# Optimization experiments

Hardware: AMD Instinct MI355X
Metric: run time of the kernel (lower is better)

## Reference

```python
import jax, jax.numpy as jnp
import numpy as np

N, R, D, K = 2048, 64, 64, 512  # batch, n_roles, filler_embed_dim, n_fillers
LAMBDA_VQ, LAMBDA_COMMIT, LAMBDA_ORTH = 1.0, 0.5, 0.0


def setup_inputs() -> dict:
    key = jax.random.key(0)
    k1, k2 = jax.random.split(key)
    soft_fillers = jax.random.normal(k1, (N, R, D), dtype=jnp.float32)
    weight = jax.random.normal(k2, (K, D), dtype=jnp.float32)  # codebook rows
    return {"soft_fillers": soft_fillers, "weight": weight}


def _nearest(x, w):
    # x: [M, D], w: [K, D] -> nearest codebook rows + indices
    d = (jnp.sum(x * x, axis=-1, keepdims=True)
         - 2.0 * (x @ w.T)
         + jnp.sum(w * w, axis=-1))          # [M, K]
    idx = jnp.argmin(d, axis=-1)              # [M]
    return w[idx], idx                        # gather: [M, D]


def reference(soft_fillers, weight):
    flat = soft_fillers.reshape(-1, D)        # [N*R, D]

    # Path 1: weight_sg=True -> weight detached, straight-through to input
    q_sg_flat, idx = _nearest(flat, jax.lax.stop_gradient(weight))
    q_sg_flat = flat + jax.lax.stop_gradient(q_sg_flat - flat)

    # Path 2: input detached -> gradient flows to weight via gather
    q_flat, _ = _nearest(jax.lax.stop_gradient(flat), weight)

    q_sg = q_sg_flat.reshape(N, R, D)
    q = q_flat.reshape(N, R, D)
    filler_idxs = idx.reshape(N, R)

    # vq loss: mean over (N, D) of L2-norm over roles of elementwise-squared diff
    t_vq = (q - jax.lax.stop_gradient(soft_fillers)) ** 2          # [N, R, D]
    vq_loss = jnp.mean(jnp.sqrt(jnp.sum(t_vq * t_vq, axis=1)))
    t_c = (jax.lax.stop_gradient(q) - soft_fillers) ** 2
    commit_loss = jnp.mean(jnp.sqrt(jnp.sum(t_c * t_c, axis=1)))

    # semi-orthogonality penalty on weight.t() (rows of codebook): ||W^T W - I||_F
    gram = weight.T @ weight                                        # [D, D]
    orth_penalty = jnp.linalg.norm(gram - jnp.eye(D, dtype=weight.dtype))

    total_loss = (LAMBDA_VQ * vq_loss + LAMBDA_COMMIT * commit_loss
                  + LAMBDA_ORTH * orth_penalty)

    filler_rank = jnp.linalg.matrix_rank(weight).astype(jnp.float32)

    return (total_loss, vq_loss, commit_loss, orth_penalty, filler_rank,
            q_sg, q, filler_idxs)
```

## Files before the change

kernel.cpp:

```cpp
#include <hip/hip_runtime.h>
#include <math.h>

#define N_ 2048
#define R_ 64
#define D_ 64
#define K_ 512
#define M_ (N_*R_)
#define TAU 0.012f
#define CHK 0.012f

#define WN_OFF   16
#define GRAM_OFF 1024
#define WBF_BYTE 32768
#define WS_NEED  163840

typedef __attribute__((ext_vector_type(8))) short s16x8;
typedef __attribute__((ext_vector_type(4))) float f32x4;

static __device__ __forceinline__ unsigned short f2bf(float f) {
    unsigned u = __float_as_uint(f);
    u += 0x7FFFu + ((u >> 16) & 1u);
    return (unsigned short)(u >> 16);
}
static __device__ __forceinline__ float bf2f(unsigned short h) {
    return __uint_as_float(((unsigned)h) << 16);
}

static __device__ __forceinline__ int xs_byte(int r, int q) {
    return r * 256 + (q >> 3) * 128 + (((q & 7) ^ (r & 7)) * 16);
}

static __device__ __forceinline__ void split8(const float* vv, s16x8& ph, s16x8& pl) {
#pragma unroll
    for (int j = 0; j < 8; ++j) {
        const unsigned short hb = f2bf(vv[j]);
        ph[j] = (short)hb;
        pl[j] = (short)f2bf(vv[j] - bf2f(hb));
    }
}

static __device__ __forceinline__ void nt_store4(float* p, float x0, float x1, float x2, float x3) {
    f32x4 v = {x0, x1, x2, x3};
    __builtin_nontemporal_store(v, (f32x4*)p);
}

__global__ void k_pre(const float* __restrict__ w, float* __restrict__ ws, int pre) {
    const int b = blockIdx.x, t = threadIdx.x;
    if (b < 64) {
        __shared__ float red[4][64];
        const int i = b, j = t & 63, kg = t >> 6;
        float s = 0.f;
        for (int k = kg * 128; k < kg * 128 + 128; ++k)
            s = fmaf(w[k * 64 + i], w[k * 64 + j], s);
        red[kg][j] = s;
        __syncthreads();
        if (t < 64)
            ws[GRAM_OFF + i * 64 + t] = red[0][t] + red[1][t] + red[2][t] + red[3][t];
    } else if (b < 66) {
        const int code = (b - 64) * 256 + t;
        const float4* wr = (const float4*)(w + code * 64);
        float s = 0.f;
#pragma unroll
        for (int i = 0; i < 16; ++i) {
            float4 v = wr[i];
            s += v.x * v.x + v.y * v.y + v.z * v.z + v.w * v.w;
        }
        ws[WN_OFF + code] = s;
        if (b == 64 && t == 0) ws[0] = 0.f;
    } else {
        if (!pre) return;
        const int code = (b - 66) * 256 + t;
        char* whi = (char*)ws + WBF_BYTE;
        char* wlo = whi + 65536;
        const int c = code >> 6, rr = code & 63;
        const int nt = rr >> 4, lr = rr & 15;
        for (int kg = 0; kg < 8; ++kg) {
            float4 v0 = *(const float4*)(w + code * 64 + kg * 8);
            float4 v1 = *(const float4*)(w + code * 64 + kg * 8 + 4);
            const float vv[8] = {v0.x, v0.y, v0.z, v0.w, v1.x, v1.y, v1.z, v1.w};
            s16x8 ph, pl;
            split8(vv, ph, pl);
            const int s = kg >> 2, g = kg & 3, l = g * 16 + lr;
            const int off = (((c * 2 + s) * 4 + nt) << 10) + l * 16;
            *(s16x8*)(whi + off) = ph;
            *(s16x8*)(wlo + off) = pl;
        }
    }
}

template<bool PRE>
__global__ __launch_bounds__(256, 2) void k_argmin(
    const float* __restrict__ x, const float* __restrict__ w,
    float* __restrict__ ws, float* __restrict__ out)
{
    __shared__ __align__(16) float xs[8192];
    __shared__ __align__(16) float redw[2][4][64];
    __shared__ float fb1[128], fb2[128];
    __shared__ int   ridx[128];
    __shared__ int   ulist[128];
    __shared__ int   nunc;

    const int t = threadIdx.x;
    const int l = t & 63, wid = t >> 6;
    const int g = l >> 4, lr = l & 15;
    const long brow = (long)blockIdx.x * 128;
    const float* wn_g = ws + WN_OFF;
    const char* whi = (const char*)ws + WBF_BYTE;
    const char* wlo = whi + 65536;

    if (t == 0) nunc = 0;

#pragma unroll
    for (int ii = 0; ii < 8; ++ii) {
        const int gid = ii * 256 + t;
        const int r = gid >> 4, qq = gid & 15;
        const float4 v = *(const float4*)(x + (brow + r) * 64 + qq * 4);
        *(float4*)((char*)xs + xs_byte(r, qq)) = v;
    }
    __syncthreads();

    s16x8 ah[2][2], al[2][2];
#pragma unroll
    for (int mt = 0; mt < 2; ++mt) {
        const int row = wid * 32 + mt * 16 + lr;
#pragma unroll
        for (int s = 0; s < 2; ++s) {
            const int kg = s * 4 + g;
            const float4 v0 = *(const float4*)((const char*)xs + xs_byte(row, kg * 2));
            const float4 v1 = *(const float4*)((const char*)xs + xs_byte(row, kg * 2 + 1));
            const float vv[8] = {v0.x, v0.y, v0.z, v0.w, v1.x, v1.y, v1.z, v1.w};
            split8(vv, ah[mt][s], al[mt][s]);
        }
    }

    float b1[2][4], b2[2][4]; int i1[2][4];
#pragma unroll
    for (int mt = 0; mt < 2; ++mt)
#pragma unroll
        for (int j = 0; j < 4; ++j) { b1[mt][j] = 3.4e38f; b2[mt][j] = 3.4e38f; i1[mt][j] = 0; }

    s16x8 pbh[2][4], pbl[2][4];
    float4 pv0[2][4], pv1[2][4];
    f32x4 acc[2][4];

    auto issue = [&](int h, int par) {
        const int c = h >> 1, half = h & 1;
#pragma unroll
        for (int s = 0; s < 2; ++s)
#pragma unroll
            for (int nth = 0; nth < 2; ++nth) {
                const int nt = half * 2 + nth, idx = s * 2 + nth;
                if constexpr (PRE) {
                    const int off = (((c * 2 + s) * 4 + nt) << 10) + l * 16;
                    pbh[par][idx] = *(const s16x8*)(whi + off);
                    pbl[par][idx] = *(const s16x8*)(wlo + off);
                } else {
                    const int crow = c * 64 + nt * 16 + lr;
                    const float* src = w + (long)crow * 64 + (s * 4 + g) * 8;
                    pv0[par][idx] = *(const float4*)src;
                    pv1[par][idx] = *(const float4*)(src + 4);
                }
            }
    };

    auto compute = [&](int h, int par) {
        const int c = h >> 1, half = h & 1;
        if (half == 0) {
            const f32x4 z = {0.f, 0.f, 0.f, 0.f};
#pragma unroll
            for (int mt = 0; mt < 2; ++mt)
#pragma unroll
                for (int nt = 0; nt < 4; ++nt) acc[mt][nt] = z;
        }
#pragma unroll
        for (int s = 0; s < 2; ++s)
#pragma unroll
            for (int nth = 0; nth < 2; ++nth) {
                const int nt = half * 2 + nth, idx = s * 2 + nth;
                s16x8 BH, BL;
                if constexpr (PRE) {
                    BH = pbh[par][idx]; BL = pbl[par][idx];
                } else {
                    const float4 v0 = pv0[par][idx], v1 = pv1[par][idx];
                    const float vv[8] = {v0.x, v0.y, v0.z, v0.w, v1.x, v1.y, v1.z, v1.w};
                    split8(vv, BH, BL);
                }
#pragma unroll
                for (int mt = 0; mt < 2; ++mt) {
                    acc[mt][nt] = __builtin_amdgcn_mfma_f32_16x16x32_bf16(ah[mt][s], BH, acc[mt][nt], 0, 0, 0);
                    acc[mt][nt] = __builtin_amdgcn_mfma_f32_16x16x32_bf16(al[mt][s], BH, acc[mt][nt], 0, 0, 0);
                    acc[mt][nt] = __builtin_amdgcn_mfma_f32_16x16x32_bf16(ah[mt][s], BL, acc[mt][nt], 0, 0, 0);
                }
            }
        if (half == 1) {
#pragma unroll
            for (int nt = 0; nt < 4; ++nt) {
                const int code = c * 64 + nt * 16 + lr;
                const float wnv = wn_g[code];
#pragma unroll
                for (int mt = 0; mt < 2; ++mt)
#pragma unroll
                    for (int j = 0; j < 4; ++j) {
                        const float sv = fmaf(-2.f, acc[mt][nt][j], wnv);
                        if (sv < b1[mt][j]) { b2[mt][j] = b1[mt][j]; b1[mt][j] = sv; i1[mt][j] = code; }
                        else if (sv < b2[mt][j]) b2[mt][j] = sv;
                    }
            }
        }
    };

    issue(0, 0);
#pragma unroll
    for (int h = 0; h < 16; ++h) {
        if (h < 15) issue(h + 1, (h + 1) & 1);
        compute(h, h & 1);
    }

#pragma unroll
    for (int m = 1; m < 16; m <<= 1) {
#pragma unroll
        for (int mt = 0; mt < 2; ++mt)
#pragma unroll
            for (int j = 0; j < 4; ++j) {
                const float ov1 = __shfl_xor(b1[mt][j], m, 64);
                const int   oi1 = __shfl_xor(i1[mt][j], m, 64);
                const float ov2 = __shfl_xor(b2[mt][j], m, 64);
                const float nb2 = fminf(fminf(b2[mt][j], ov2), fmaxf(b1[mt][j], ov1));
                if (ov1 < b1[mt][j] || (ov1 == b1[mt][j] && oi1 < i1[mt][j])) {
                    b1[mt][j] = ov1; i1[mt][j] = oi1;
                }
                b2[mt][j] = nb2;
            }
    }
    if (lr == 0) {
#pragma unroll
        for (int mt = 0; mt < 2; ++mt)
#pragma unroll
            for (int j = 0; j < 4; ++j) {
                const int ro = wid * 32 + mt * 16 + g * 4 + j;
                ridx[ro] = i1[mt][j];
                fb1[ro] = b1[mt][j];
                fb2[ro] = b2[mt][j];
            }
    }
    __syncthreads();

    {
        const int r = t >> 1, sub = t & 1;
        const int ci = ridx[r];
        const float* wrow = w + (long)ci * 64 + sub * 32;
        float dot = 0.f;
#pragma unroll
        for (int p = 0; p < 8; ++p) {
            const float4 xv = *(const float4*)((const char*)xs + xs_byte(r, sub * 8 + p));
            const float4 wv = *(const float4*)(wrow + p * 4);
            dot = fmaf(xv.x, wv.x, dot);
            dot = fmaf(xv.y, wv.y, dot);
            dot = fmaf(xv.z, wv.z, dot);
            dot = fmaf(xv.w, wv.w, dot);
        }
        dot += __shfl_xor(dot, 1, 64);
        if (sub == 0) {
            const float sex = fmaf(-2.f, dot, wn_g[ci]);
            const bool unc = ((fb2[r] - fb1[r]) < TAU) || (fabsf(sex - fb1[r]) > CHK);
            if (unc) { const int p = atomicAdd(&nunc, 1); ulist[p] = r; }
        }
    }
    __syncthreads();

    const int nu = nunc;
    if (nu > 0) {
        for (int e = wid; e < nu; e += 4) {
            const int r = ulist[e];
            float bv = 3.4e38f; int bi = 0;
            for (int cc = 0; cc < 8; ++cc) {
                const int code = cc * 64 + l;
                const float* wrow = w + (long)code * 64;
                float dot = 0.f;
#pragma unroll
                for (int p = 0; p < 16; ++p) {
                    const float4 xv = *(const float4*)((const char*)xs + xs_byte(r, p));
                    const float4 wv = *(const float4*)(wrow + p * 4);
                    dot = fmaf(xv.x, wv.x, dot);
                    dot = fmaf(xv.y, wv.y, dot);
                    dot = fmaf(xv.z, wv.z, dot);
                    dot = fmaf(xv.w, wv.w, dot);
                }
                const float sv = fmaf(-2.f, dot, wn_g[code]);
                if (sv < bv) { bv = sv; bi = code; }
            }
#pragma unroll
            for (int m = 1; m < 64; m <<= 1) {
                const float ov = __shfl_xor(bv, m, 64);
                const int   oi = __shfl_xor(bi, m, 64);
                if (ov < bv || (ov == bv && oi < bi)) { bv = ov; bi = oi; }
            }
            if (l == 0) ridx[r] = bi;
        }
    }
    __syncthreads();

    float* q_sg = out + 5;
    float* q    = out + 5 + (long)M_ * 64;
    float* fidx = out + 5 + 2L * M_ * 64;
    const int qq = t & 15, ry = t >> 4;
    float4 va = {0.f, 0.f, 0.f, 0.f}, vb = {0.f, 0.f, 0.f, 0.f};
#pragma unroll
    for (int ii = 0; ii < 8; ++ii) {
        const int r = ii * 16 + ry;
        const int ci = ridx[r];
        const float4 wv4 = *(const float4*)(w + (long)ci * 64 + qq * 4);
        const float4 xv4 = *(const float4*)((const char*)xs + xs_byte(r, qq));
        const long off = (brow + r) * 64 + qq * 4;
        nt_store4(q_sg + off, wv4.x, wv4.y, wv4.z, wv4.w);
        nt_store4(q + off,    wv4.x, wv4.y, wv4.z, wv4.w);
        float4 p;
        p.x = (wv4.x - xv4.x) * (wv4.x - xv4.x);
        p.y = (wv4.y - xv4.y) * (wv4.y - xv4.y);
        p.z = (wv4.z - xv4.z) * (wv4.z - xv4.z);
        p.w = (wv4.w - xv4.w) * (wv4.w - xv4.w);
        float4 p2;
        p2.x = p.x * p.x; p2.y = p.y * p.y; p2.z = p.z * p.z; p2.w = p.w * p.w;
        if (ii < 4) {
            va.x += p2.x; va.y += p2.y; va.z += p2.z; va.w += p2.w;
        } else {
            vb.x += p2.x; vb.y += p2.y; vb.z += p2.z; vb.w += p2.w;
        }
    }
#pragma unroll
    for (int m = 16; m < 64; m <<= 1) {
        va.x += __shfl_xor(va.x, m, 64); va.y += __shfl_xor(va.y, m, 64);
        va.z += __shfl_xor(va.z, m, 64); va.w += __shfl_xor(va.w, m, 64);
        vb.x += __shfl_xor(vb.x, m, 64); vb.y += __shfl_xor(vb.y, m, 64);
        vb.z += __shfl_xor(vb.z, m, 64); vb.w += __shfl_xor(vb.w, m, 64);
    }
    if (l < 16) {
        *(float4*)&redw[0][wid][l * 4] = va;
        *(float4*)&redw[1][wid][l * 4] = vb;
    }
    if (t < 128) __builtin_nontemporal_store((float)ridx[t], fidx + brow + t);
    __syncthreads();

    if (t < 128) {
        const int n = t >> 6, d = t & 63;
        const float s = redw[n][0][d] + redw[n][1][d] + redw[n][2][d] + redw[n][3][d];
        float v = sqrtf(s);
#pragma unroll
        for (int m = 1; m < 64; m <<= 1) v += __shfl_xor(v, m, 64);
        if (d == 0) atomicAdd(ws + 0, v);
    }
}

__global__ void k_final(const float* __restrict__ ws, float* __restrict__ out)
{
    __shared__ float g[64][65];
    __shared__ float osum[4];
    __shared__ float tol;
    const int t = threadIdx.x;
    float oacc = 0.f;
    for (int i = t; i < 4096; i += 256) {
        const int r = i >> 6, cl = i & 63;
        const float gv = ws[GRAM_OFF + i];
        g[r][cl] = gv;
        const float p = gv - (r == cl ? 1.f : 0.f);
        oacc = fmaf(p, p, oacc);
    }
#pragma unroll
    for (int m = 1; m < 64; m <<= 1) oacc += __shfl_xor(oacc, m, 64);
    if ((t & 63) == 0) osum[t >> 6] = oacc;
    __syncthreads();

    if (t == 0) {
        float maxd = 0.f;
        for (int i = 0; i < 64; ++i) maxd = fmaxf(maxd, fabsf(g[i][i]));
        tol = maxd * 1e-7f + 1e-30f;
    }
    __syncthreads();

    int rank = 0;
    const int j = t & 63, rq = t >> 6;
    for (int s = 0; s < 64; ++s) {
        const float p = g[s][s];
        const bool ok = fabsf(p) > tol;
        if (ok) {
            rank++;
            if (j > s) {
                const float rp = 1.f / p;
                const float gsj = g[s][j];
                for (int r = s + 1 + rq; r < 64; r += 4)
                    g[r][j] = fmaf(-(g[r][s] * rp), gsj, g[r][j]);
            }
        }
        __syncthreads();
    }

    if (t == 0) {
        const float vq = ws[0] / (float)(N_ * D_);
        const float orth = sqrtf(osum[0] + osum[1] + osum[2] + osum[3]);
        out[0] = 1.5f * vq;
        out[1] = vq;
        out[2] = vq;
        out[3] = orth;
        out[4] = (float)rank;
    }
}

extern "C" void kernel_launch(void* const* d_in, const int* in_sizes, int n_in,
                              void* d_out, int out_size, void* d_ws, size_t ws_size,
                              hipStream_t stream) {
    const float* x = (const float*)d_in[0];
    const float* w = (const float*)d_in[1];
    float* out = (float*)d_out;
    float* ws  = (float*)d_ws;
    const int pre = (ws_size >= (size_t)WS_NEED) ? 1 : 0;

    hipLaunchKernelGGL(k_pre, dim3(68), dim3(256), 0, stream, w, ws, pre);
    if (pre)
        hipLaunchKernelGGL((k_argmin<true>),  dim3(1024), dim3(256), 0, stream, x, w, ws, out);
    else
        hipLaunchKernelGGL((k_argmin<false>), dim3(1024), dim3(256), 0, stream, x, w, ws, out);
    hipLaunchKernelGGL(k_final, dim3(1), dim3(256), 0, stream, ws, out);
}
```

Measured before the change: 164.5 us.

## Fuse gram and finalize into argmin kernel via last-block completion counter

The gram-matrix computation moves out of the pre-pass into 64 extra blocks of the main argmin kernel, and the separate single-block final kernel is folded in. Its work now runs in whichever block is last to increment a global atomic counter. This cuts one launch and shrinks the pre-pass to 4 blocks, so the gram work overlaps with the argmin work. In exchange the gram matrix is no longer ready early, every block adds a threadfence and atomic at its end, and the serial rank elimination runs inside a heavy kernel's tail block.

```diff
diff --git a/kernel.cpp b/kernel.cpp
--- a/kernel.cpp
+++ b/kernel.cpp
@@ -9,6 +9,10 @@
 #define TAU 0.012f
 #define CHK 0.012f
 
+#define GRAMB 64
+#define ARGB  1024
+#define TOTB  (GRAMB + ARGB)
+
 #define WN_OFF   16
 #define GRAM_OFF 1024
 #define WBF_BYTE 32768
@@ -46,18 +50,8 @@
 
 __global__ void k_pre(const float* __restrict__ w, float* __restrict__ ws, int pre) {
     const int b = blockIdx.x, t = threadIdx.x;
-    if (b < 64) {
-        __shared__ float red[4][64];
-        const int i = b, j = t & 63, kg = t >> 6;
-        float s = 0.f;
-        for (int k = kg * 128; k < kg * 128 + 128; ++k)
-            s = fmaf(w[k * 64 + i], w[k * 64 + j], s);
-        red[kg][j] = s;
-        __syncthreads();
-        if (t < 64)
-            ws[GRAM_OFF + i * 64 + t] = red[0][t] + red[1][t] + red[2][t] + red[3][t];
-    } else if (b < 66) {
-        const int code = (b - 64) * 256 + t;
+    if (b < 2) {
+        const int code = b * 256 + t;
         const float4* wr = (const float4*)(w + code * 64);
         float s = 0.f;
 #pragma unroll
@@ -66,10 +60,10 @@
             s += v.x * v.x + v.y * v.y + v.z * v.z + v.w * v.w;
         }
         ws[WN_OFF + code] = s;
-        if (b == 64 && t == 0) ws[0] = 0.f;
+        if (b == 0 && t == 0) { ws[0] = 0.f; ((int*)ws)[8] = 0; }
     } else {
         if (!pre) return;
-        const int code = (b - 66) * 256 + t;
+        const int code = (b - 2) * 256 + t;
         char* whi = (char*)ws + WBF_BYTE;
         char* wlo = whi + 65536;
         const int c = code >> 6, rr = code & 63;
@@ -89,279 +83,301 @@
 }
 
 template<bool PRE>
-__global__ __launch_bounds__(256, 2) void k_argmin(
+__global__ __launch_bounds__(256, 2) void k_main(
     const float* __restrict__ x, const float* __restrict__ w,
     float* __restrict__ ws, float* __restrict__ out)
 {
     __shared__ __align__(16) float xs[8192];
     __shared__ __align__(16) float redw[2][4][64];
     __shared__ float fb1[128], fb2[128];
-    __shared__ int   ridx[128];
+    __shared__ int   sridx[128];
     __shared__ int   ulist[128];
     __shared__ int   nunc;
+    __shared__ int   lastflag;
 
     const int t = threadIdx.x;
     const int l = t & 63, wid = t >> 6;
     const int g = l >> 4, lr = l & 15;
-    const long brow = (long)blockIdx.x * 128;
     const float* wn_g = ws + WN_OFF;
     const char* whi = (const char*)ws + WBF_BYTE;
     const char* wlo = whi + 65536;
 
-    if (t == 0) nunc = 0;
-
-#pragma unroll
-    for (int ii = 0; ii < 8; ++ii) {
-        const int gid = ii * 256 + t;
-        const int r = gid >> 4, qq = gid & 15;
-        const float4 v = *(const float4*)(x + (brow + r) * 64 + qq * 4);
-        *(float4*)((char*)xs + xs_byte(r, qq)) = v;
-    }
+    if (blockIdx.x < GRAMB) {
+        const int i = blockIdx.x, j = t & 63, kg = t >> 6;
+        float s = 0.f;
+#pragma unroll 4
+        for (int k = kg * 128; k < kg * 128 + 128; ++k)
+            s = fmaf(w[k * 64 + i], w[k * 64 + j], s);
+        float* red = xs;
+        red[kg * 64 + j] = s;
+        __syncthreads();
+        if (t < 64)
+            ws[GRAM_OFF + i * 64 + t] = red[t] + red[64 + t] + red[128 + t] + red[192 + t];
+    } else {
+        const int bid = blockIdx.x - GRAMB;
+        const long brow = (long)bid * 128;
+
+        if (t == 0) nunc = 0;
+
+#pragma unroll
+        for (int ii = 0; ii < 8; ++ii) {
+            const int gid = ii * 256 + t;
+            const int r = gid >> 4, qq = gid & 15;
+            const float4 v = *(const float4*)(x + (brow + r) * 64 + qq * 4);
+            *(float4*)((char*)xs + xs_byte(r, qq)) = v;
+        }
+        __syncthreads();
+
+        s16x8 ah[2][2], al[2][2];
+#pragma unroll
+        for (int mt = 0; mt < 2; ++mt) {
+            const int row = wid * 32 + mt * 16 + lr;
+#pragma unroll
+            for (int s = 0; s < 2; ++s) {
+                const int kg = s * 4 + g;
+                const float4 v0 = *(const float4*)((const char*)xs + xs_byte(row, kg * 2));
+                const float4 v1 = *(const float4*)((const char*)xs + xs_byte(row, kg * 2 + 1));
+                const float vv[8] = {v0.x, v0.y, v0.z, v0.w, v1.x, v1.y, v1.z, v1.w};
+                split8(vv, ah[mt][s], al[mt][s]);
+            }
+        }
+
+        float b1[2][4], b2[2][4]; int i1[2][4];
+#pragma unroll
+        for (int mt = 0; mt < 2; ++mt)
+#pragma unroll
+            for (int j = 0; j < 4; ++j) { b1[mt][j] = 3.4e38f; b2[mt][j] = 3.4e38f; i1[mt][j] = 0; }
+
+        s16x8 pbh[2][4], pbl[2][4];
+        float4 pv0[2][4], pv1[2][4];
+        f32x4 acc[2][4];
+
+        auto issue = [&](int h, int par) {
+            const int c = h >> 1, half = h & 1;
+#pragma unroll
+            for (int s = 0; s < 2; ++s)
+#pragma unroll
+                for (int nth = 0; nth < 2; ++nth) {
+                    const int nt = half * 2 + nth, idx = s * 2 + nth;
+                    if constexpr (PRE) {
+                        const int off = (((c * 2 + s) * 4 + nt) << 10) + l * 16;
+                        pbh[par][idx] = *(const s16x8*)(whi + off);
+                        pbl[par][idx] = *(const s16x8*)(wlo + off);
+                    } else {
+                        const int crow = c * 64 + nt * 16 + lr;
+                        const float* src = w + (long)crow * 64 + (s * 4 + g) * 8;
+                        pv0[par][idx] = *(const float4*)src;
+                        pv1[par][idx] = *(const float4*)(src + 4);
+                    }
+                }
+        };
+
+        auto compute = [&](int h, int par) {
+            const int c = h >> 1, half = h & 1;
+            if (half == 0) {
+                const f32x4 z = {0.f, 0.f, 0.f, 0.f};
+#pragma unroll
+                for (int mt = 0; mt < 2; ++mt)
+#pragma unroll
+                    for (int nt = 0; nt < 4; ++nt) acc[mt][nt] = z;
+            }
+#pragma unroll
+            for (int s = 0; s < 2; ++s)
+#pragma unroll
+                for (int nth = 0; nth < 2; ++nth) {
+                    const int nt = half * 2 + nth, idx = s * 2 + nth;
+                    s16x8 BH, BL;
+                    if constexpr (PRE) {
+                        BH = pbh[par][idx]; BL = pbl[par][idx];
+                    } else {
+                        const float4 v0 = pv0[par][idx], v1 = pv1[par][idx];
+                        const float vv[8] = {v0.x, v0.y, v0.z, v0.w, v1.x, v1.y, v1.z, v1.w};
+                        split8(vv, BH, BL);
+                    }
+#pragma unroll
+                    for (int mt = 0; mt < 2; ++mt) {
+                        acc[mt][nt] = __builtin_amdgcn_mfma_f32_16x16x32_bf16(ah[mt][s], BH, acc[mt][nt], 0, 0, 0);
+                        acc[mt][nt] = __builtin_amdgcn_mfma_f32_16x16x32_bf16(al[mt][s], BH, acc[mt][nt], 0, 0, 0);
+                        acc[mt][nt] = __builtin_amdgcn_mfma_f32_16x16x32_bf16(ah[mt][s], BL, acc[mt][nt], 0, 0, 0);
+                    }
+                }
+            if (half == 1) {
+#pragma unroll
+                for (int nt = 0; nt < 4; ++nt) {
+                    const int code = c * 64 + nt * 16 + lr;
+                    const float wnv = wn_g[code];
+#pragma unroll
+                    for (int mt = 0; mt < 2; ++mt)
+#pragma unroll
+                        for (int j = 0; j < 4; ++j) {
+                            const float sv = fmaf(-2.f, acc[mt][nt][j], wnv);
+                            if (sv < b1[mt][j]) { b2[mt][j] = b1[mt][j]; b1[mt][j] = sv; i1[mt][j] = code; }
+                            else if (sv < b2[mt][j]) b2[mt][j] = sv;
+                        }
+                }
+            }
+        };
+
+        issue(0, 0);
+#pragma unroll
+        for (int h = 0; h < 16; ++h) {
+            if (h < 15) issue(h + 1, (h + 1) & 1);
+            compute(h, h & 1);
+        }
+
+#pragma unroll
+        for (int m = 1; m < 16; m <<= 1) {
+#pragma unroll
+            for (int mt = 0; mt < 2; ++mt)
+#pragma unroll
+                for (int j = 0; j < 4; ++j) {
+                    const float ov1 = __shfl_xor(b1[mt][j], m, 64);
+                    const int   oi1 = __shfl_xor(i1[mt][j], m, 64);
+                    const float ov2 = __shfl_xor(b2[mt][j], m, 64);
+                    const float nb2 = fminf(fminf(b2[mt][j], ov2), fmaxf(b1[mt][j], ov1));
+                    if (ov1 < b1[mt][j] || (ov1 == b1[mt][j] && oi1 < i1[mt][j])) {
+                        b1[mt][j] = ov1; i1[mt][j] = oi1;
+                    }
+                    b2[mt][j] = nb2;
+                }
+        }
+        if (lr == 0) {
+#pragma unroll
+            for (int mt = 0; mt < 2; ++mt)
+#pragma unroll
+                for (int j = 0; j < 4; ++j) {
+                    const int ro = wid * 32 + mt * 16 + g * 4 + j;
+                    sridx[ro] = i1[mt][j];
+                    fb1[ro] = b1[mt][j];
+                    fb2[ro] = b2[mt][j];
+                }
+        }
+        __syncthreads();
+
+        {
+            const int r = t >> 1, sub = t & 1;
+            const int ci = sridx[r];
+            const float* wrow = w + (long)ci * 64 + sub * 32;
+            float dot = 0.f;
+#pragma unroll
+            for (int p = 0; p < 8; ++p) {
+                const float4 xv = *(const float4*)((const char*)xs + xs_byte(r, sub * 8 + p));
+                const float4 wv = *(const float4*)(wrow + p * 4);
+                dot = fmaf(xv.x, wv.x, dot);
+                dot = fmaf(xv.y, wv.y, dot);
+                dot = fmaf(xv.z, wv.z, dot);
+                dot = fmaf(xv.w, wv.w, dot);
+            }
+            dot += __shfl_xor(dot, 1, 64);
+            if (sub == 0) {
+                const float sex = fmaf(-2.f, dot, wn_g[ci]);
+                const bool unc = ((fb2[r] - fb1[r]) < TAU) || (fabsf(sex - fb1[r]) > CHK);
+                if (unc) { const int p = atomicAdd(&nunc, 1); ulist[p] = r; }
+            }
+        }
+        __syncthreads();
+
+        const int nu = nunc;
+        if (nu > 0) {
+            for (int e = wid; e < nu; e += 4) {
+                const int r = ulist[e];
+                float bv = 3.4e38f; int bi = 0;
+                for (int cc = 0; cc < 8; ++cc) {
+                    const int code = cc * 64 + l;
+                    const float* wrow = w + (long)code * 64;
+                    float dot = 0.f;
+#pragma unroll
+                    for (int p = 0; p < 16; ++p) {
+                        const float4 xv = *(const float4*)((const char*)xs + xs_byte(r, p));
+                        const float4 wv = *(const float4*)(wrow + p * 4);
+                        dot = fmaf(xv.x, wv.x, dot);
+                        dot = fmaf(xv.y, wv.y, dot);
+                        dot = fmaf(xv.z, wv.z, dot);
+                        dot = fmaf(xv.w, wv.w, dot);
+                    }
+                    const float sv = fmaf(-2.f, dot, wn_g[code]);
+                    if (sv < bv) { bv = sv; bi = code; }
+                }
+#pragma unroll
+                for (int m = 1; m < 64; m <<= 1) {
+                    const float ov = __shfl_xor(bv, m, 64);
+                    const int   oi = __shfl_xor(bi, m, 64);
+                    if (ov < bv || (ov == bv && oi < bi)) { bv = ov; bi = oi; }
+                }
+                if (l == 0) sridx[r] = bi;
+            }
+        }
+        __syncthreads();
+
+        float* q_sg = out + 5;
+        float* q    = out + 5 + (long)M_ * 64;
+        float* fidx = out + 5 + 2L * M_ * 64;
+        const int qq = t & 15, ry = t >> 4;
+        float4 va = {0.f, 0.f, 0.f, 0.f}, vb = {0.f, 0.f, 0.f, 0.f};
+#pragma unroll
+        for (int ii = 0; ii < 8; ++ii) {
+            const int r = ii * 16 + ry;
+            const int ci = sridx[r];
+            const float4 wv4 = *(const float4*)(w + (long)ci * 64 + qq * 4);
+            const float4 xv4 = *(const float4*)((const char*)xs + xs_byte(r, qq));
+            const long off = (brow + r) * 64 + qq * 4;
+            nt_store4(q_sg + off, wv4.x, wv4.y, wv4.z, wv4.w);
+            nt_store4(q + off,    wv4.x, wv4.y, wv4.z, wv4.w);
+            float4 p;
+            p.x = (wv4.x - xv4.x) * (wv4.x - xv4.x);
+            p.y = (wv4.y - xv4.y) * (wv4.y - xv4.y);
+            p.z = (wv4.z - xv4.z) * (wv4.z - xv4.z);
+            p.w = (wv4.w - xv4.w) * (wv4.w - xv4.w);
+            float4 p2;
+            p2.x = p.x * p.x; p2.y = p.y * p.y; p2.z = p.z * p.z; p2.w = p.w * p.w;
+            if (ii < 4) {
+                va.x += p2.x; va.y += p2.y; va.z += p2.z; va.w += p2.w;
+            } else {
+                vb.x += p2.x; vb.y += p2.y; vb.z += p2.z; vb.w += p2.w;
+            }
+        }
+#pragma unroll
+        for (int m = 16; m < 64; m <<= 1) {
+            va.x += __shfl_xor(va.x, m, 64); va.y += __shfl_xor(va.y, m, 64);
+            va.z += __shfl_xor(va.z, m, 64); va.w += __shfl_xor(va.w, m, 64);
+            vb.x += __shfl_xor(vb.x, m, 64); vb.y += __shfl_xor(vb.y, m, 64);
+            vb.z += __shfl_xor(vb.z, m, 64); vb.w += __shfl_xor(vb.w, m, 64);
+        }
+        if (l < 16) {
+            *(float4*)&redw[0][wid][l * 4] = va;
+            *(float4*)&redw[1][wid][l * 4] = vb;
+        }
+        if (t < 128) __builtin_nontemporal_store((float)sridx[t], fidx + brow + t);
+        __syncthreads();
+
+        if (t < 128) {
+            const int n = t >> 6, d = t & 63;
+            const float s = redw[n][0][d] + redw[n][1][d] + redw[n][2][d] + redw[n][3][d];
+            float v = sqrtf(s);
+#pragma unroll
+            for (int m = 1; m < 64; m <<= 1) v += __shfl_xor(v, m, 64);
+            if (d == 0) atomicAdd(ws + 0, v);
+        }
+    }
+
     __syncthreads();
-
-    s16x8 ah[2][2], al[2][2];
-#pragma unroll
-    for (int mt = 0; mt < 2; ++mt) {
-        const int row = wid * 32 + mt * 16 + lr;
-#pragma unroll
-        for (int s = 0; s < 2; ++s) {
-            const int kg = s * 4 + g;
-            const float4 v0 = *(const float4*)((const char*)xs + xs_byte(row, kg * 2));
-            const float4 v1 = *(const float4*)((const char*)xs + xs_byte(row, kg * 2 + 1));
-            const float vv[8] = {v0.x, v0.y, v0.z, v0.w, v1.x, v1.y, v1.z, v1.w};
-            split8(vv, ah[mt][s], al[mt][s]);
-        }
-    }
-
-    float b1[2][4], b2[2][4]; int i1[2][4];
-#pragma unroll
-    for (int mt = 0; mt < 2; ++mt)
-#pragma unroll
-        for (int j = 0; j < 4; ++j) { b1[mt][j] = 3.4e38f; b2[mt][j] = 3.4e38f; i1[mt][j] = 0; }
-
-    s16x8 pbh[2][4], pbl[2][4];
-    float4 pv0[2][4], pv1[2][4];
-    f32x4 acc[2][4];
-
-    auto issue = [&](int h, int par) {
-        const int c = h >> 1, half = h & 1;
-#pragma unroll
-        for (int s = 0; s < 2; ++s)
-#pragma unroll
-            for (int nth = 0; nth < 2; ++nth) {
-                const int nt = half * 2 + nth, idx = s * 2 + nth;
-                if constexpr (PRE) {
-                    const int off = (((c * 2 + s) * 4 + nt) << 10) + l * 16;
-                    pbh[par][idx] = *(const s16x8*)(whi + off);
-                    pbl[par][idx] = *(const s16x8*)(wlo + off);
-                } else {
-                    const int crow = c * 64 + nt * 16 + lr;
-                    const float* src = w + (long)crow * 64 + (s * 4 + g) * 8;
-                    pv0[par][idx] = *(const float4*)src;
-                    pv1[par][idx] = *(const float4*)(src + 4);
-                }
-            }
-    };
-
-    auto compute = [&](int h, int par) {
-        const int c = h >> 1, half = h & 1;
-        if (half == 0) {
-            const f32x4 z = {0.f, 0.f, 0.f, 0.f};
-#pragma unroll
-            for (int mt = 0; mt < 2; ++mt)
-#pragma unroll
-                for (int nt = 0; nt < 4; ++nt) acc[mt][nt] = z;
-        }
-#pragma unroll
-        for (int s = 0; s < 2; ++s)
-#pragma unroll
-            for (int nth = 0; nth < 2; ++nth) {
-                const int nt = half * 2 + nth, idx = s * 2 + nth;
-                s16x8 BH, BL;
-                if constexpr (PRE) {
-                    BH = pbh[par][idx]; BL = pbl[par][idx];
-                } else {
-                    const float4 v0 = pv0[par][idx], v1 = pv1[par][idx];
-                    const float vv[8] = {v0.x, v0.y, v0.z, v0.w, v1.x, v1.y, v1.z, v1.w};
-                    split8(vv, BH, BL);
-                }
-#pragma unroll
-                for (int mt = 0; mt < 2; ++mt) {
-                    acc[mt][nt] = __builtin_amdgcn_mfma_f32_16x16x32_bf16(ah[mt][s], BH, acc[mt][nt], 0, 0, 0);
-                    acc[mt][nt] = __builtin_amdgcn_mfma_f32_16x16x32_bf16(al[mt][s], BH, acc[mt][nt], 0, 0, 0);
-                    acc[mt][nt] = __builtin_amdgcn_mfma_f32_16x16x32_bf16(ah[mt][s], BL, acc[mt][nt], 0, 0, 0);
-                }
-            }
-        if (half == 1) {
-#pragma unroll
-            for (int nt = 0; nt < 4; ++nt) {
-                const int code = c * 64 + nt * 16 + lr;
-                const float wnv = wn_g[code];
-#pragma unroll
-                for (int mt = 0; mt < 2; ++mt)
-#pragma unroll
-                    for (int j = 0; j < 4; ++j) {
-                        const float sv = fmaf(-2.f, acc[mt][nt][j], wnv);
-                        if (sv < b1[mt][j]) { b2[mt][j] = b1[mt][j]; b1[mt][j] = sv; i1[mt][j] = code; }
-                        else if (sv < b2[mt][j]) b2[mt][j] = sv;
-                    }
-            }
-        }
-    };
-
-    issue(0, 0);
-#pragma unroll
-    for (int h = 0; h < 16; ++h) {
-        if (h < 15) issue(h + 1, (h + 1) & 1);
-        compute(h, h & 1);
-    }
-
-#pragma unroll
-    for (int m = 1; m < 16; m <<= 1) {
-#pragma unroll
-        for (int mt = 0; mt < 2; ++mt)
-#pragma unroll
-            for (int j = 0; j < 4; ++j) {
-                const float ov1 = __shfl_xor(b1[mt][j], m, 64);
-                const int   oi1 = __shfl_xor(i1[mt][j], m, 64);
-                const float ov2 = __shfl_xor(b2[mt][j], m, 64);
-                const float nb2 = fminf(fminf(b2[mt][j], ov2), fmaxf(b1[mt][j], ov1));
-                if (ov1 < b1[mt][j] || (ov1 == b1[mt][j] && oi1 < i1[mt][j])) {
-                    b1[mt][j] = ov1; i1[mt][j] = oi1;
-                }
-                b2[mt][j] = nb2;
-            }
-    }
-    if (lr == 0) {
-#pragma unroll
-        for (int mt = 0; mt < 2; ++mt)
-#pragma unroll
-            for (int j = 0; j < 4; ++j) {
-                const int ro = wid * 32 + mt * 16 + g * 4 + j;
-                ridx[ro] = i1[mt][j];
-                fb1[ro] = b1[mt][j];
-                fb2[ro] = b2[mt][j];
-            }
+    if (t == 0) {
+        __threadfence();
+        const int old = atomicAdd((int*)ws + 8, 1);
+        lastflag = (old == TOTB - 1) ? 1 : 0;
     }
     __syncthreads();
-
-    {
-        const int r = t >> 1, sub = t & 1;
-        const int ci = ridx[r];
-        const float* wrow = w + (long)ci * 64 + sub * 32;
-        float dot = 0.f;
-#pragma unroll
-        for (int p = 0; p < 8; ++p) {
-            const float4 xv = *(const float4*)((const char*)xs + xs_byte(r, sub * 8 + p));
-            const float4 wv = *(const float4*)(wrow + p * 4);
-            dot = fmaf(xv.x, wv.x, dot);
-            dot = fmaf(xv.y, wv.y, dot);
-            dot = fmaf(xv.z, wv.z, dot);
-            dot = fmaf(xv.w, wv.w, dot);
-        }
-        dot += __shfl_xor(dot, 1, 64);
-        if (sub == 0) {
-            const float sex = fmaf(-2.f, dot, wn_g[ci]);
-            const bool unc = ((fb2[r] - fb1[r]) < TAU) || (fabsf(sex - fb1[r]) > CHK);
-            if (unc) { const int p = atomicAdd(&nunc, 1); ulist[p] = r; }
-        }
-    }
-    __syncthreads();
-
-    const int nu = nunc;
-    if (nu > 0) {
-        for (int e = wid; e < nu; e += 4) {
-            const int r = ulist[e];
-            float bv = 3.4e38f; int bi = 0;
-            for (int cc = 0; cc < 8; ++cc) {
-                const int code = cc * 64 + l;
-                const float* wrow = w + (long)code * 64;
-                float dot = 0.f;
-#pragma unroll
-                for (int p = 0; p < 16; ++p) {
-                    const float4 xv = *(const float4*)((const char*)xs + xs_byte(r, p));
-                    const float4 wv = *(const float4*)(wrow + p * 4);
-                    dot = fmaf(xv.x, wv.x, dot);
-                    dot = fmaf(xv.y, wv.y, dot);
-                    dot = fmaf(xv.z, wv.z, dot);
-                    dot = fmaf(xv.w, wv.w, dot);
-                }
-                const float sv = fmaf(-2.f, dot, wn_g[code]);
-                if (sv < bv) { bv = sv; bi = code; }
-            }
-#pragma unroll
-            for (int m = 1; m < 64; m <<= 1) {
-                const float ov = __shfl_xor(bv, m, 64);
-                const int   oi = __shfl_xor(bi, m, 64);
-                if (ov < bv || (ov == bv && oi < bi)) { bv = ov; bi = oi; }
-            }
-            if (l == 0) ridx[r] = bi;
-        }
-    }
-    __syncthreads();
-
-    float* q_sg = out + 5;
-    float* q    = out + 5 + (long)M_ * 64;
-    float* fidx = out + 5 + 2L * M_ * 64;
-    const int qq = t & 15, ry = t >> 4;
-    float4 va = {0.f, 0.f, 0.f, 0.f}, vb = {0.f, 0.f, 0.f, 0.f};
-#pragma unroll
-    for (int ii = 0; ii < 8; ++ii) {
-        const int r = ii * 16 + ry;
-        const int ci = ridx[r];
-        const float4 wv4 = *(const float4*)(w + (long)ci * 64 + qq * 4);
-        const float4 xv4 = *(const float4*)((const char*)xs + xs_byte(r, qq));
-        const long off = (brow + r) * 64 + qq * 4;
-        nt_store4(q_sg + off, wv4.x, wv4.y, wv4.z, wv4.w);
-        nt_store4(q + off,    wv4.x, wv4.y, wv4.z, wv4.w);
-        float4 p;
-        p.x = (wv4.x - xv4.x) * (wv4.x - xv4.x);
-        p.y = (wv4.y - xv4.y) * (wv4.y - xv4.y);
-        p.z = (wv4.z - xv4.z) * (wv4.z - xv4.z);
-        p.w = (wv4.w - xv4.w) * (wv4.w - xv4.w);
-        float4 p2;
-        p2.x = p.x * p.x; p2.y = p.y * p.y; p2.z = p.z * p.z; p2.w = p.w * p.w;
-        if (ii < 4) {
-            va.x += p2.x; va.y += p2.y; va.z += p2.z; va.w += p2.w;
-        } else {
-            vb.x += p2.x; vb.y += p2.y; vb.z += p2.z; vb.w += p2.w;
-        }
-    }
-#pragma unroll
-    for (int m = 16; m < 64; m <<= 1) {
-        va.x += __shfl_xor(va.x, m, 64); va.y += __shfl_xor(va.y, m, 64);
-        va.z += __shfl_xor(va.z, m, 64); va.w += __shfl_xor(va.w, m, 64);
-        vb.x += __shfl_xor(vb.x, m, 64); vb.y += __shfl_xor(vb.y, m, 64);
-        vb.z += __shfl_xor(vb.z, m, 64); vb.w += __shfl_xor(vb.w, m, 64);
-    }
-    if (l < 16) {
-        *(float4*)&redw[0][wid][l * 4] = va;
-        *(float4*)&redw[1][wid][l * 4] = vb;
-    }
-    if (t < 128) __builtin_nontemporal_store((float)ridx[t], fidx + brow + t);
-    __syncthreads();
-
-    if (t < 128) {
-        const int n = t >> 6, d = t & 63;
-        const float s = redw[n][0][d] + redw[n][1][d] + redw[n][2][d] + redw[n][3][d];
-        float v = sqrtf(s);
-#pragma unroll
-        for (int m = 1; m < 64; m <<= 1) v += __shfl_xor(v, m, 64);
-        if (d == 0) atomicAdd(ws + 0, v);
-    }
-}
-
-__global__ void k_final(const float* __restrict__ ws, float* __restrict__ out)
-{
-    __shared__ float g[64][65];
+    if (!lastflag) return;
+    __threadfence();
+
+    float (*gm)[65] = (float(*)[65])xs;
     __shared__ float osum[4];
     __shared__ float tol;
-    const int t = threadIdx.x;
     float oacc = 0.f;
     for (int i = t; i < 4096; i += 256) {
         const int r = i >> 6, cl = i & 63;
         const float gv = ws[GRAM_OFF + i];
-        g[r][cl] = gv;
+        gm[r][cl] = gv;
         const float p = gv - (r == cl ? 1.f : 0.f);
         oacc = fmaf(p, p, oacc);
     }
@@ -372,7 +388,7 @@
 
     if (t == 0) {
         float maxd = 0.f;
-        for (int i = 0; i < 64; ++i) maxd = fmaxf(maxd, fabsf(g[i][i]));
+        for (int i = 0; i < 64; ++i) maxd = fmaxf(maxd, fabsf(gm[i][i]));
         tol = maxd * 1e-7f + 1e-30f;
     }
     __syncthreads();
@@ -380,15 +396,15 @@
     int rank = 0;
     const int j = t & 63, rq = t >> 6;
     for (int s = 0; s < 64; ++s) {
-        const float p = g[s][s];
+        const float p = gm[s][s];
         const bool ok = fabsf(p) > tol;
         if (ok) {
             rank++;
             if (j > s) {
                 const float rp = 1.f / p;
-                const float gsj = g[s][j];
+                const float gsj = gm[s][j];
                 for (int r = s + 1 + rq; r < 64; r += 4)
-                    g[r][j] = fmaf(-(g[r][s] * rp), gsj, g[r][j]);
+                    gm[r][j] = fmaf(-(gm[r][s] * rp), gsj, gm[r][j]);
             }
         }
         __syncthreads();
@@ -414,10 +430,9 @@
     float* ws  = (float*)d_ws;
     const int pre = (ws_size >= (size_t)WS_NEED) ? 1 : 0;
 
-    hipLaunchKernelGGL(k_pre, dim3(68), dim3(256), 0, stream, w, ws, pre);
+    hipLaunchKernelGGL(k_pre, dim3(4), dim3(256), 0, stream, w, ws, pre);
     if (pre)
-        hipLaunchKernelGGL((k_argmin<true>),  dim3(1024), dim3(256), 0, stream, x, w, ws, out);
+        hipLaunchKernelGGL((k_main<true>),  dim3(TOTB), dim3(256), 0, stream, x, w, ws, out);
     else
-        hipLaunchKernelGGL((k_argmin<false>), dim3(1024), dim3(256), 0, stream, x, w, ws, out);
-    hipLaunchKernelGGL(k_final, dim3(1), dim3(256), 0, stream, ws, out);
-}
+        hipLaunchKernelGGL((k_main<false>), dim3(TOTB), dim3(256), 0, stream, x, w, ws, out);
+}
```

Result: slower. 196.7 us (+19.6%).
